# Optimization experiments

Measured on AMD Instinct MI355X. Metric: run time of the kernel, lower is better.

The kernel has to match this reference:

```python
import jax, jax.numpy as jnp
import numpy as np

BATCH, SEQ, STATE, D_IN, D_OUT = 32, 8192, 128, 128, 128


def setup_inputs() -> dict:
    key = jax.random.key(0)
    k1, k2, k3, k4, k5 = jax.random.split(key, 5)
    A = jnp.tril(jax.random.normal(k1, (STATE, STATE), dtype=jnp.float32) * 0.01)
    B = jax.random.normal(k2, (STATE, D_IN), dtype=jnp.float32) * 0.01
    C = jax.random.normal(k3, (D_OUT, STATE), dtype=jnp.float32) * 0.01
    D = jax.random.normal(k4, (D_OUT, D_IN), dtype=jnp.float32) * 0.01
    u = jax.random.normal(k5, (BATCH, SEQ, D_IN), dtype=jnp.float32)
    return {"u": u, "A": A, "B": B, "C": C, "D": D}


def reference(u, A, B, C, D):
    # u: [b, L, d_in]; A: [S, S] (lower-tri); B: [S, d_in]; C: [d_out, S]; D: [d_out, d_in]
    S = A.shape[0]
    Bu = jnp.einsum('bld,sd->bls', u, B)                      # [b, L, S]
    I_minus_A = jnp.eye(S, dtype=u.dtype) - A                 # [S, S], lower-tri
    # Solve (I - A) x = Bu^T. The matrix is shared across batch and time, so
    # fold (b, L) into one rhs-column axis: one trsm instead of b batched solves.
    rhs = Bu.reshape(-1, S).T                                 # [S, b*L]
    x = jax.scipy.linalg.solve_triangular(I_minus_A, rhs, lower=True)  # [S, b*L]
    x_seq = x.T.reshape(Bu.shape)                             # [b, L, S]
    y = jnp.einsum('bls,os->blo', x_seq, C) + jnp.einsum('bld,od->blo', u, D)
    return y
```

## Files before the change

### kernel.cpp

```cpp
#include <hip/hip_runtime.h>
#include <stdint.h>

typedef __attribute__((ext_vector_type(8))) short bf16x8;
typedef __attribute__((ext_vector_type(4))) float f32x4;

static __device__ __forceinline__ uint16_t f2bf(float f) {
    uint32_t u;
    __builtin_memcpy(&u, &f, 4);
    return (uint16_t)((u + 0x7FFFu + ((u >> 16) & 1u)) >> 16);
}

__global__ __launch_bounds__(64) void k1_solve(const float* __restrict__ Ag,
                                               const float* __restrict__ Bg,
                                               float* __restrict__ X) {
    __shared__ float Ap[16 * 128];
    __shared__ float Bp[16 * 64];
    __shared__ float xT[64 * 128];

    const int dl = threadIdx.x;
    const int d  = blockIdx.x * 64 + dl;
    const int sw = (dl & 7) << 2;
    float* xrow = &xT[dl * 128];

    for (int p = 0; p < 8; ++p) {
        __syncthreads();
        {
            const f32x4* src = reinterpret_cast<const f32x4*>(Ag + p * 2048);
            f32x4* dst = reinterpret_cast<f32x4*>(Ap);
#pragma unroll
            for (int i = 0; i < 8; ++i) dst[i * 64 + dl] = src[i * 64 + dl];
#pragma unroll
            for (int i = 0; i < 16; ++i) Bp[i * 64 + dl] = Bg[(p * 16 + i) * 128 + d];
        }
        __syncthreads();

        for (int sl = 0; sl < 16; ++sl) {
            const int s = p * 16 + sl;
            const float* Ar = Ap + sl * 128;
            float a0 = 0.f, a1 = 0.f, a2 = 0.f, a3 = 0.f;
            const int nq = s >> 2;
            for (int q = 0; q < nq; ++q) {
                f32x4 av = *reinterpret_cast<const f32x4*>(Ar + q * 4);
                f32x4 xv = *reinterpret_cast<const f32x4*>(xrow + ((q * 4) ^ sw));
                a0 += av[0] * xv[0];
                a1 += av[1] * xv[1];
                a2 += av[2] * xv[2];
                a3 += av[3] * xv[3];
            }
            float acc = (a0 + a1) + (a2 + a3);
            for (int t = nq * 4; t < s; ++t) acc += Ar[t] * xrow[t ^ sw];
            float xs = (Bp[sl * 64 + dl] + acc) / (1.0f - Ar[s]);
            xrow[s ^ sw] = xs;
            X[s * 128 + d] = xs;
        }
    }
}

__global__ __launch_bounds__(128) void k2_makeM(const float* __restrict__ X,
                                                const float* __restrict__ Cg,
                                                const float* __restrict__ Dg,
                                                uint16_t* __restrict__ Mfrag) {
    const int o = blockIdx.x;
    const int d = threadIdx.x;
    float a0 = 0.f, a1 = 0.f, a2 = 0.f, a3 = 0.f;
#pragma unroll
    for (int s = 0; s < 128; s += 4) {
        a0 += Cg[o * 128 + s + 0] * X[(s + 0) * 128 + d];
        a1 += Cg[o * 128 + s + 1] * X[(s + 1) * 128 + d];
        a2 += Cg[o * 128 + s + 2] * X[(s + 2) * 128 + d];
        a3 += Cg[o * 128 + s + 3] * X[(s + 3) * 128 + d];
    }
    float m = ((a0 + a1) + (a2 + a3)) + Dg[o * 128 + d];

    const int c = o >> 4, n = o & 15;
    const int t = d >> 5, r = d & 31;
    const int half = r >> 3, j = r & 7;
    const int lane = half * 16 + n;
    const int f = c * 4 + t;
    Mfrag[(f * 64 + lane) * 8 + j] = f2bf(m);
}

__global__ __launch_bounds__(256, 4) void k3_gemm(const float* __restrict__ U,
                                                  const uint16_t* __restrict__ Mfrag,
                                                  float* __restrict__ Y) {
    __shared__ uint16_t Msh[16384];
    {
        const uint4* src = reinterpret_cast<const uint4*>(Mfrag);
        uint4* dst = reinterpret_cast<uint4*>(Msh);
#pragma unroll
        for (int i = 0; i < 8; ++i)
            dst[threadIdx.x + 256 * i] = src[threadIdx.x + 256 * i];
    }
    __syncthreads();

    const int lane = threadIdx.x & 63;
    const int wid  = threadIdx.x >> 6;
    const int urow = lane & 15;
    const int kh   = lane >> 4;

    const int rowbase = blockIdx.x * 64 + wid * 16;

    const float* up = U + (size_t)(rowbase + urow) * 128 + kh * 8;
    bf16x8 Afr[4];
#pragma unroll
    for (int t = 0; t < 4; ++t) {
        f32x4 lo = *reinterpret_cast<const f32x4*>(up + t * 32);
        f32x4 hi = *reinterpret_cast<const f32x4*>(up + t * 32 + 4);
        bf16x8 a;
#pragma unroll
        for (int j = 0; j < 4; ++j) {
            a[j]     = (short)f2bf(lo[j]);
            a[4 + j] = (short)f2bf(hi[j]);
        }
        Afr[t] = a;
    }

    f32x4 acc[8] = {};
#pragma unroll
    for (int c = 0; c < 8; ++c) {
#pragma unroll
        for (int t = 0; t < 4; ++t) {
            bf16x8 b = *reinterpret_cast<const bf16x8*>(Msh + ((c * 4 + t) * 64 + lane) * 8);
            acc[c] = __builtin_amdgcn_mfma_f32_16x16x32_bf16(b, Afr[t], acc[c], 0, 0, 0);
        }
    }

    float* yp = Y + (size_t)(rowbase + urow) * 128 + kh * 4;
#pragma unroll
    for (int c = 0; c < 8; ++c)
        *reinterpret_cast<f32x4*>(yp + c * 16) = acc[c];
}

extern "C" void kernel_launch(void* const* d_in, const int* in_sizes, int n_in,
                              void* d_out, int out_size, void* d_ws, size_t ws_size,
                              hipStream_t stream) {
    const float* u = (const float*)d_in[0];
    const float* A = (const float*)d_in[1];
    const float* B = (const float*)d_in[2];
    const float* C = (const float*)d_in[3];
    const float* D = (const float*)d_in[4];

    float*    X     = (float*)d_ws;
    uint16_t* Mfrag = (uint16_t*)((char*)d_ws + 65536);
    float*    Y     = (float*)d_out;

    hipLaunchKernelGGL(k1_solve, dim3(2),    dim3(64),  0, stream, A, B, X);
    hipLaunchKernelGGL(k2_makeM, dim3(128),  dim3(128), 0, stream, X, C, D, Mfrag);
    hipLaunchKernelGGL(k3_gemm,  dim3(4096), dim3(256), 0, stream, u, Mfrag, Y);
}
```

Measured before the change: 317.9 us.

## Fuse solve and M construction into one kernel; software-pipeline GEMM over four row tiles

```diff
diff --git a/kernel.cpp b/kernel.cpp
--- a/kernel.cpp
+++ b/kernel.cpp
@@ -10,16 +10,19 @@
     return (uint16_t)((u + 0x7FFFu + ((u >> 16) & 1u)) >> 16);
 }
 
-__global__ __launch_bounds__(64) void k1_solve(const float* __restrict__ Ag,
-                                               const float* __restrict__ Bg,
-                                               float* __restrict__ X) {
+__global__ __launch_bounds__(128) void k12_solve_makeM(const float* __restrict__ Ag,
+                                                       const float* __restrict__ Bg,
+                                                       const float* __restrict__ Cg,
+                                                       const float* __restrict__ Dg,
+                                                       uint16_t* __restrict__ Mfrag) {
     __shared__ float Ap[16 * 128];
     __shared__ float Bp[16 * 64];
     __shared__ float xT[64 * 128];
 
-    const int dl = threadIdx.x;
-    const int d  = blockIdx.x * 64 + dl;
-    const int sw = (dl & 7) << 2;
+    const int tid = threadIdx.x;
+    const int dl  = tid & 63;
+    const int d   = blockIdx.x * 64 + dl;
+    const int sw  = (dl & 7) << 2;
     float* xrow = &xT[dl * 128];
 
     for (int p = 0; p < 8; ++p) {
@@ -28,56 +31,86 @@
             const f32x4* src = reinterpret_cast<const f32x4*>(Ag + p * 2048);
             f32x4* dst = reinterpret_cast<f32x4*>(Ap);
 #pragma unroll
-            for (int i = 0; i < 8; ++i) dst[i * 64 + dl] = src[i * 64 + dl];
+            for (int i = 0; i < 4; ++i) dst[i * 128 + tid] = src[i * 128 + tid];
 #pragma unroll
-            for (int i = 0; i < 16; ++i) Bp[i * 64 + dl] = Bg[(p * 16 + i) * 128 + d];
+            for (int w = 0; w < 8; ++w) {
+                int idx = w * 128 + tid;
+                int row = idx >> 6, col = idx & 63;
+                Bp[idx] = Bg[(p * 16 + row) * 128 + blockIdx.x * 64 + col];
+            }
         }
         __syncthreads();
 
-        for (int sl = 0; sl < 16; ++sl) {
-            const int s = p * 16 + sl;
-            const float* Ar = Ap + sl * 128;
-            float a0 = 0.f, a1 = 0.f, a2 = 0.f, a3 = 0.f;
-            const int nq = s >> 2;
-            for (int q = 0; q < nq; ++q) {
-                f32x4 av = *reinterpret_cast<const f32x4*>(Ar + q * 4);
+        if (tid < 64) {
+            float base[16];
+#pragma unroll
+            for (int i = 0; i < 16; ++i) base[i] = 0.f;
+            for (int q = 0; q < 4 * p; ++q) {
                 f32x4 xv = *reinterpret_cast<const f32x4*>(xrow + ((q * 4) ^ sw));
-                a0 += av[0] * xv[0];
-                a1 += av[1] * xv[1];
-                a2 += av[2] * xv[2];
-                a3 += av[3] * xv[3];
+#pragma unroll
+                for (int i = 0; i < 16; ++i) {
+                    f32x4 av = *reinterpret_cast<const f32x4*>(Ap + i * 128 + q * 4);
+                    base[i] += av[0] * xv[0] + av[1] * xv[1] + av[2] * xv[2] + av[3] * xv[3];
+                }
             }
-            float acc = (a0 + a1) + (a2 + a3);
-            for (int t = nq * 4; t < s; ++t) acc += Ar[t] * xrow[t ^ sw];
-            float xs = (Bp[sl * 64 + dl] + acc) / (1.0f - Ar[s]);
-            xrow[s ^ sw] = xs;
-            X[s * 128 + d] = xs;
+            const int t0 = p * 16;
+#pragma unroll
+            for (int sl = 0; sl < 16; ++sl) {
+                const int s = t0 + sl;
+                const float* Ar = Ap + sl * 128;
+                float acc = base[sl];
+#pragma unroll
+                for (int qq = 0; qq < (sl >> 2); ++qq) {
+                    int tq = t0 + qq * 4;
+                    f32x4 av = *reinterpret_cast<const f32x4*>(Ar + tq);
+                    f32x4 xv = *reinterpret_cast<const f32x4*>(xrow + (tq ^ sw));
+                    acc += av[0] * xv[0] + av[1] * xv[1] + av[2] * xv[2] + av[3] * xv[3];
+                }
+#pragma unroll
+                for (int k = 0; k < (sl & 3); ++k) {
+                    int t = t0 + (sl & ~3) + k;
+                    acc += Ar[t] * xrow[t ^ sw];
+                }
+                float xs = (Bp[sl * 64 + dl] + acc) / (1.0f - Ar[s]);
+                xrow[s ^ sw] = xs;
+            }
         }
     }
-}
 
-__global__ __launch_bounds__(128) void k2_makeM(const float* __restrict__ X,
-                                                const float* __restrict__ Cg,
-                                                const float* __restrict__ Dg,
-                                                uint16_t* __restrict__ Mfrag) {
-    const int o = blockIdx.x;
-    const int d = threadIdx.x;
-    float a0 = 0.f, a1 = 0.f, a2 = 0.f, a3 = 0.f;
+    const int oh = tid >> 6;
+    for (int ot = 0; ot < 8; ++ot) {
+        __syncthreads();
+        for (int w = tid; w < 2048; w += 128) {
+            int rr = w >> 7;
+            int cc = w & 127;
+            int o  = (rr >> 3) * 64 + ot * 8 + (rr & 7);
+            Ap[w] = Cg[o * 128 + cc];
+        }
+        __syncthreads();
+        float macc[8];
 #pragma unroll
-    for (int s = 0; s < 128; s += 4) {
-        a0 += Cg[o * 128 + s + 0] * X[(s + 0) * 128 + d];
-        a1 += Cg[o * 128 + s + 1] * X[(s + 1) * 128 + d];
-        a2 += Cg[o * 128 + s + 2] * X[(s + 2) * 128 + d];
-        a3 += Cg[o * 128 + s + 3] * X[(s + 3) * 128 + d];
+        for (int r = 0; r < 8; ++r) macc[r] = 0.f;
+        const float* Crow = Ap + oh * (8 * 128);
+        for (int q = 0; q < 32; ++q) {
+            f32x4 xv = *reinterpret_cast<const f32x4*>(xrow + ((q * 4) ^ sw));
+#pragma unroll
+            for (int r = 0; r < 8; ++r) {
+                f32x4 cv = *reinterpret_cast<const f32x4*>(Crow + r * 128 + q * 4);
+                macc[r] += cv[0] * xv[0] + cv[1] * xv[1] + cv[2] * xv[2] + cv[3] * xv[3];
+            }
+        }
+#pragma unroll
+        for (int r = 0; r < 8; ++r) {
+            const int o = oh * 64 + ot * 8 + r;
+            float m = macc[r] + Dg[o * 128 + d];
+            const int c = o >> 4, n = o & 15;
+            const int t = d >> 5, r2 = d & 31;
+            const int half = r2 >> 3, j = r2 & 7;
+            const int lane = half * 16 + n;
+            const int f = c * 4 + t;
+            Mfrag[(f * 64 + lane) * 8 + j] = f2bf(m);
+        }
     }
-    float m = ((a0 + a1) + (a2 + a3)) + Dg[o * 128 + d];
-
-    const int c = o >> 4, n = o & 15;
-    const int t = d >> 5, r = d & 31;
-    const int half = r >> 3, j = r & 7;
-    const int lane = half * 16 + n;
-    const int f = c * 4 + t;
-    Mfrag[(f * 64 + lane) * 8 + j] = f2bf(m);
 }
 
 __global__ __launch_bounds__(256, 4) void k3_gemm(const float* __restrict__ U,
@@ -98,37 +131,51 @@
     const int urow = lane & 15;
     const int kh   = lane >> 4;
 
-    const int rowbase = blockIdx.x * 64 + wid * 16;
+    const size_t wrow = (size_t)blockIdx.x * 256 + (size_t)wid * 64;
+    const float* up = U + (wrow + urow) * 128 + kh * 8;
 
-    const float* up = U + (size_t)(rowbase + urow) * 128 + kh * 8;
-    bf16x8 Afr[4];
+    f32x4 buf[8];
 #pragma unroll
     for (int t = 0; t < 4; ++t) {
-        f32x4 lo = *reinterpret_cast<const f32x4*>(up + t * 32);
-        f32x4 hi = *reinterpret_cast<const f32x4*>(up + t * 32 + 4);
-        bf16x8 a;
-#pragma unroll
-        for (int j = 0; j < 4; ++j) {
-            a[j]     = (short)f2bf(lo[j]);
-            a[4 + j] = (short)f2bf(hi[j]);
-        }
-        Afr[t] = a;
+        buf[2 * t]     = *reinterpret_cast<const f32x4*>(up + t * 32);
+        buf[2 * t + 1] = *reinterpret_cast<const f32x4*>(up + t * 32 + 4);
     }
 
-    f32x4 acc[8] = {};
 #pragma unroll
-    for (int c = 0; c < 8; ++c) {
+    for (int it = 0; it < 4; ++it) {
+        bf16x8 Afr[4];
 #pragma unroll
         for (int t = 0; t < 4; ++t) {
-            bf16x8 b = *reinterpret_cast<const bf16x8*>(Msh + ((c * 4 + t) * 64 + lane) * 8);
-            acc[c] = __builtin_amdgcn_mfma_f32_16x16x32_bf16(b, Afr[t], acc[c], 0, 0, 0);
+            f32x4 lo = buf[2 * t], hi = buf[2 * t + 1];
+            bf16x8 a;
+#pragma unroll
+            for (int j = 0; j < 4; ++j) {
+                a[j]     = (short)f2bf(lo[j]);
+                a[4 + j] = (short)f2bf(hi[j]);
+            }
+            Afr[t] = a;
         }
+        if (it < 3) {
+            const float* upn = up + (size_t)(it + 1) * 16 * 128;
+#pragma unroll
+            for (int t = 0; t < 4; ++t) {
+                buf[2 * t]     = *reinterpret_cast<const f32x4*>(upn + t * 32);
+                buf[2 * t + 1] = *reinterpret_cast<const f32x4*>(upn + t * 32 + 4);
+            }
+        }
+        f32x4 acc[8] = {};
+#pragma unroll
+        for (int c = 0; c < 8; ++c)
+#pragma unroll
+            for (int t = 0; t < 4; ++t) {
+                bf16x8 b = *reinterpret_cast<const bf16x8*>(Msh + ((c * 4 + t) * 64 + lane) * 8);
+                acc[c] = __builtin_amdgcn_mfma_f32_16x16x32_bf16(b, Afr[t], acc[c], 0, 0, 0);
+            }
+        float* yp = Y + (wrow + it * 16 + urow) * 128 + kh * 4;
+#pragma unroll
+        for (int c = 0; c < 8; ++c)
+            *reinterpret_cast<f32x4*>(yp + c * 16) = acc[c];
     }
-
-    float* yp = Y + (size_t)(rowbase + urow) * 128 + kh * 4;
-#pragma unroll
-    for (int c = 0; c < 8; ++c)
-        *reinterpret_cast<f32x4*>(yp + c * 16) = acc[c];
 }
 
 extern "C" void kernel_launch(void* const* d_in, const int* in_sizes, int n_in,
@@ -140,11 +187,9 @@
     const float* C = (const float*)d_in[3];
     const float* D = (const float*)d_in[4];
 
-    float*    X     = (float*)d_ws;
-    uint16_t* Mfrag = (uint16_t*)((char*)d_ws + 65536);
+    uint16_t* Mfrag = (uint16_t*)d_ws;
     float*    Y     = (float*)d_out;
 
-    hipLaunchKernelGGL(k1_solve, dim3(2),    dim3(64),  0, stream, A, B, X);
-    hipLaunchKernelGGL(k2_makeM, dim3(128),  dim3(128), 0, stream, X, C, D, Mfrag);
-    hipLaunchKernelGGL(k3_gemm,  dim3(4096), dim3(256), 0, stream, u, Mfrag, Y);
+    hipLaunchKernelGGL(k12_solve_makeM, dim3(2),    dim3(128), 0, stream, A, B, C, D, Mfrag);
+    hipLaunchKernelGGL(k3_gemm,         dim3(1024), dim3(256), 0, stream, u, Mfrag, Y);
 }
```

Measured after the change: 332.0 us. +4.4%, slower.
